# Kernel tuning notes

Hardware: AMD Instinct MI355X
Metric: run time of the kernel (lower is better)

## Reference

```python
import jax, jax.numpy as jnp
import numpy as np

# ---- config (from init_kwargs) ----
IMG_SIZE = (4096.0, 4096.0)
MAP_SIZE = (256, 256)
BASE_SIZE = 16
RATIOS = np.array([0.5, 1.0, 2.0], dtype=np.float64)
SCALES = np.array([8.0, 16.0, 32.0], dtype=np.float64)
FEAT_STRIDE = 16
RPN_MIN_SIZE = 16.0
PRE_NMS_N = 12000
POST_NMS_N = 2000
NMS_THRESH = 0.7


def _generate_anchors():
    base = np.array([1, 1, BASE_SIZE, BASE_SIZE], dtype=np.float64) - 1
    w = base[2] - base[0] + 1
    h = base[3] - base[1] + 1
    cx = base[0] + 0.5 * (w - 1)
    cy = base[1] + 0.5 * (h - 1)
    size = w * h
    ws = np.round(np.sqrt(size / RATIOS))
    hs = np.round(ws * RATIOS)
    ratio_anchors = np.stack([cx - 0.5 * (ws - 1), cy - 0.5 * (hs - 1),
                              cx + 0.5 * (ws - 1), cy + 0.5 * (hs - 1)], axis=1)
    out = []
    for a in ratio_anchors:
        aw = a[2] - a[0] + 1
        ah = a[3] - a[1] + 1
        acx = a[0] + 0.5 * (aw - 1)
        acy = a[1] + 0.5 * (ah - 1)
        ws2 = aw * SCALES
        hs2 = ah * SCALES
        out.append(np.stack([acx - 0.5 * (ws2 - 1), acy - 0.5 * (hs2 - 1),
                             acx + 0.5 * (ws2 - 1), acy + 0.5 * (hs2 - 1)], axis=1))
    return np.concatenate(out, axis=0).astype(np.float32)  # [A=9, 4]


def _all_anchors():
    A = _generate_anchors()
    H, W = MAP_SIZE
    sx = np.arange(W) * FEAT_STRIDE
    sy = np.arange(H) * FEAT_STRIDE
    sx, sy = np.meshgrid(sx, sy)
    shifts = np.stack([sx.ravel(), sy.ravel(), sx.ravel(), sy.ravel()], axis=1).astype(np.float32)  # [K,4]
    return (shifts[:, None, :] + A[None, :, :]).reshape(-1, 4)  # [K*A, 4]


_ALL_ANCHORS = _all_anchors()  # [N, 4] constant


def setup_inputs() -> dict:
    key = jax.random.key(0)
    k1, k2 = jax.random.split(key)
    n = _ALL_ANCHORS.shape[0]
    delta = jax.random.normal(k1, (1, n, 4), dtype=jnp.float32) * 0.1
    score = jax.random.uniform(k2, (1, n, 2), dtype=jnp.float32)
    return {"delta": delta, "score": score}


def _proposal_forward(delta, score):
    anchors = jnp.asarray(_ALL_ANCHORS)  # [N,4]
    d = delta[0]                         # [N,4]
    s = score[0, :, 1]                   # [N]

    widths = anchors[:, 2] - anchors[:, 0] + 1.0
    heights = anchors[:, 3] - anchors[:, 1] + 1.0
    ctr_x = anchors[:, 0] + 0.5 * widths
    ctr_y = anchors[:, 1] + 0.5 * heights
    pcx = d[:, 0] * widths + ctr_x
    pcy = d[:, 1] * heights + ctr_y
    pw = jnp.exp(d[:, 2]) * widths
    ph = jnp.exp(d[:, 3]) * heights
    x0 = jnp.clip(pcx - 0.5 * pw, 0.0, IMG_SIZE[0])
    y0 = jnp.clip(pcy - 0.5 * ph, 0.0, IMG_SIZE[1])
    x1 = jnp.clip(pcx + 0.5 * pw, 0.0, IMG_SIZE[0])
    y1 = jnp.clip(pcy + 0.5 * ph, 0.0, IMG_SIZE[1])
    props = jnp.stack([x0, y0, x1, y1], axis=1)  # [N,4]

    # min-size filter: mask instead of dynamic gather (jit-friendly)
    w = props[:, 2] - props[:, 0]
    h = props[:, 3] - props[:, 1]
    valid = (w >= RPN_MIN_SIZE) & (h >= RPN_MIN_SIZE)
    s = jnp.where(valid, s, -jnp.inf)

    top_s, top_i = jax.lax.top_k(s, PRE_NMS_N)   # sorted descending
    boxes = props[top_i]                          # [PRE,4]

    # greedy NMS over score-sorted boxes, fixed POST_NMS_N iterations
    areas = (boxes[:, 2] - boxes[:, 0]) * (boxes[:, 3] - boxes[:, 1])
    alive0 = top_s > -jnp.inf

    def step(alive, _):
        i = jnp.argmax(jnp.where(alive, top_s, -jnp.inf))
        ok = alive[i]
        b = boxes[i]
        xx0 = jnp.maximum(b[0], boxes[:, 0])
        yy0 = jnp.maximum(b[1], boxes[:, 1])
        xx1 = jnp.minimum(b[2], boxes[:, 2])
        yy1 = jnp.minimum(b[3], boxes[:, 3])
        inter = jnp.maximum(xx1 - xx0, 0.0) * jnp.maximum(yy1 - yy0, 0.0)
        iou = inter / jnp.maximum(areas[i] + areas - inter, 1e-8)
        alive = alive & (iou <= NMS_THRESH)
        out = jnp.where(ok, b, jnp.zeros_like(b))  # zero-pad like tf.pad
        return alive, out

    _, selected = jax.lax.scan(step, alive0, None, length=POST_NMS_N)  # [POST,4]
    return selected[None]  # [1, POST_NMS_N, 4]


def reference(delta, score):
    return _proposal_forward(delta, score)
```

## Files before the change

kernel.cpp:

```cpp
#include <hip/hip_runtime.h>
#include <hip/hip_bf16.h>

#define N_ANCH   589824
#define NBLK     2304
#define TOPK     12000
#define KPAD     12032
#define NW       188
#define OUTN     2000
#define CAP      32768

typedef unsigned long long u64;

__constant__ float c_aw[9] = {184.f, 368.f, 736.f, 128.f, 256.f, 512.f,  88.f, 176.f, 352.f};
__constant__ float c_ah[9] = { 96.f, 192.f, 384.f, 128.f, 256.f, 512.f, 176.f, 352.f, 704.f};

__device__ __forceinline__ void decode_one(int i, const float4* __restrict__ delta,
                                           float4* box, bool* valid) {
#pragma clang fp contract(off)
    int a    = i % 9;
    int cell = i / 9;
    int gx = cell & 255;
    int gy = cell >> 8;
    float w = c_aw[a], h = c_ah[a];
    float cx = (float)gx * 16.0f + 8.0f;
    float cy = (float)gy * 16.0f + 8.0f;
    float4 d = delta[i];
    float pcx = d.x * w + cx;
    float pcy = d.y * h + cy;
    float pw  = expf(d.z) * w;
    float ph  = expf(d.w) * h;
    float x0 = fminf(fmaxf(pcx - 0.5f * pw, 0.f), 4096.f);
    float y0 = fminf(fmaxf(pcy - 0.5f * ph, 0.f), 4096.f);
    float x1 = fminf(fmaxf(pcx + 0.5f * pw, 0.f), 4096.f);
    float y1 = fminf(fmaxf(pcy + 0.5f * ph, 0.f), 4096.f);
    *box = make_float4(x0, y0, x1, y1);
    *valid = (x1 - x0 >= 16.f) && (y1 - y0 >= 16.f);
}

__global__ __launch_bounds__(256) void k_score(const float4* __restrict__ delta,
                                               const float2* __restrict__ score,
                                               unsigned* __restrict__ ukey,
                                               unsigned* __restrict__ hist1) {
    __shared__ unsigned lh[256];
    int tid = threadIdx.x;
    lh[tid] = 0u;
    __syncthreads();
    int i = blockIdx.x * 256 + tid;
    float4 box; bool valid;
    decode_one(i, delta, &box, &valid);
    unsigned u = 0u;
    if (valid) {
        unsigned b = __float_as_uint(score[i].y);
        u = (b & 0x80000000u) ? ~b : (b | 0x80000000u);
    }
    ukey[i] = u;
    atomicAdd(&lh[u >> 24], 1u);
    __syncthreads();
    unsigned c = lh[tid];
    if (c) atomicAdd(&hist1[tid], c);
}

__global__ __launch_bounds__(256) void k_hist2(const unsigned* __restrict__ ukey,
                                               const unsigned* __restrict__ hist1,
                                               unsigned* __restrict__ hist2) {
    __shared__ unsigned ss[256];
    __shared__ unsigned lh[256];
    __shared__ unsigned s_b1;
    int tid = threadIdx.x;
    ss[tid] = hist1[tid];
    lh[tid] = 0u;
    if (tid == 0) s_b1 = 0u;
    __syncthreads();
    for (int d = 1; d < 256; d <<= 1) {
        unsigned v = (tid + d < 256) ? ss[tid + d] : 0u;
        __syncthreads();
        ss[tid] += v;
        __syncthreads();
    }
    if (ss[tid] >= (unsigned)TOPK && (tid == 255 || ss[tid + 1] < (unsigned)TOPK))
        s_b1 = (unsigned)tid;
    __syncthreads();
    unsigned b1 = s_b1;
    int i = blockIdx.x * 256 + tid;
    unsigned u = ukey[i];
    if ((u >> 24) == b1) atomicAdd(&lh[(u >> 16) & 255u], 1u);
    __syncthreads();
    unsigned c = lh[tid];
    if (c) atomicAdd(&hist2[tid], c);
}

__global__ __launch_bounds__(256) void k_compact(const unsigned* __restrict__ ukey,
                                                 const unsigned* __restrict__ hist1,
                                                 const unsigned* __restrict__ hist2,
                                                 unsigned* __restrict__ cnt,
                                                 u64* __restrict__ cand) {
    __shared__ unsigned ss[256];
    __shared__ unsigned s_b1, s_ab1, s_P;
    int tid = threadIdx.x;
    ss[tid] = hist1[tid];
    if (tid == 0) { s_b1 = 0u; s_ab1 = 0u; }
    __syncthreads();
    for (int d = 1; d < 256; d <<= 1) {
        unsigned v = (tid + d < 256) ? ss[tid + d] : 0u;
        __syncthreads();
        ss[tid] += v;
        __syncthreads();
    }
    if (ss[tid] >= (unsigned)TOPK && (tid == 255 || ss[tid + 1] < (unsigned)TOPK)) {
        s_b1 = (unsigned)tid;
        s_ab1 = (tid == 255) ? 0u : ss[tid + 1];
    }
    __syncthreads();
    unsigned b1 = s_b1, ab1 = s_ab1;
    ss[tid] = hist2[tid];
    if (tid == 0) s_P = (b1 << 8);
    __syncthreads();
    for (int d = 1; d < 256; d <<= 1) {
        unsigned v = (tid + d < 256) ? ss[tid + d] : 0u;
        __syncthreads();
        ss[tid] += v;
        __syncthreads();
    }
    unsigned target = (unsigned)TOPK - ab1;
    if (ss[tid] >= target && (tid == 255 || ss[tid + 1] < target))
        s_P = (b1 << 8) | (unsigned)tid;
    __syncthreads();
    unsigned P = s_P;

    int i = blockIdx.x * 256 + tid;
    unsigned u = ukey[i];
    bool pred = (u != 0u) && ((u >> 16) >= P);
    u64 m = __ballot(pred);
    if (m == 0ull) return;
    int lane = tid & 63;
    int leader = __ffsll(m) - 1;
    unsigned base = 0;
    if (lane == leader) base = atomicAdd(cnt, (unsigned)__popcll(m));
    base = __shfl(base, leader);
    if (pred) {
        u64 below = m & ((1ull << lane) - 1ull);
        unsigned pos = base + (unsigned)__popcll(below);
        if (pos < CAP) cand[pos] = ((u64)u << 32) | (unsigned)(~i);
    }
}

__global__ __launch_bounds__(256) void k_rankdec(const u64* __restrict__ cand,
                                                 const unsigned* __restrict__ ctrl,
                                                 const float4* __restrict__ delta,
                                                 float4* __restrict__ sboxes) {
    unsigned cnt = ctrl[3];
    int C = (int)(cnt < (unsigned)CAP ? cnt : (unsigned)CAP);
    if ((int)(blockIdx.x * 256) >= C) return;
    int t = blockIdx.x * 256 + threadIdx.x;
    u64 mykey = (t < C) ? cand[t] : ~0ull;
    int rank = 0;
    __shared__ u64 tile[256];
    for (int j0 = 0; j0 < C; j0 += 256) {
        int j = j0 + threadIdx.x;
        tile[threadIdx.x] = (j < C) ? cand[j] : 0ull;
        __syncthreads();
        int lim = (C - j0 < 256) ? (C - j0) : 256;
        #pragma unroll 4
        for (int jj = 0; jj < lim; ++jj) rank += (tile[jj] > mykey) ? 1 : 0;
        __syncthreads();
    }
    if (t < C && rank < TOPK) {
        int idx = (int)(~(unsigned)mykey);
        float4 box; bool v;
        decode_one(idx, delta, &box, &v);
        sboxes[rank] = box;
    }
}

__global__ __launch_bounds__(64) void k_mask(const float4* __restrict__ sboxes,
                                             u64* __restrict__ mcol) {
    int rb = blockIdx.y;
    int cb0 = blockIdx.x * 4;
    if (cb0 + 3 < rb) return;
    int tid = threadIdx.x;
    int r = rb * 64 + tid;
    float4 me = sboxes[r];
    float areaMe = (me.z - me.x) * (me.w - me.y);
    __shared__ float4 cbox[64];
    for (int q = 0; q < 4; ++q) {
        int cb = cb0 + q;
        if (cb < rb) continue;
        __syncthreads();
        cbox[tid] = sboxes[cb * 64 + tid];
        __syncthreads();
        u64 bits = 0ull;
        for (int j = 0; j < 64; ++j) {
            float4 o = cbox[j];
            float xx0 = fmaxf(me.x, o.x);
            float yy0 = fmaxf(me.y, o.y);
            float xx1 = fminf(me.z, o.z);
            float yy1 = fminf(me.w, o.w);
            float iw = fmaxf(xx1 - xx0, 0.f);
            float ih = fmaxf(yy1 - yy0, 0.f);
            float inter = iw * ih;
            float areaO = (o.z - o.x) * (o.w - o.y);
            float denom = fmaxf(areaMe + areaO - inter, 1e-8f);
            float iou = inter / denom;
            if (iou > 0.7f && (cb * 64 + j) != r) bits |= (1ull << j);
        }
        mcol[(size_t)cb * KPAD + r] = bits;
    }
}

__global__ __launch_bounds__(256) void k_reduce(const float4* __restrict__ sboxes,
                                                const unsigned* __restrict__ ctrl,
                                                const u64* __restrict__ mcol,
                                                float4* __restrict__ out) {
    int t = threadIdx.x;
    int lane = t & 63;
    int wave = t >> 6;
    unsigned cnt = ctrl[3];
    int C = (int)(cnt < (unsigned)CAP ? cnt : (unsigned)CAP);
    int nvalid = C < TOPK ? C : TOPK;
    int nblocks = (nvalid + 63) >> 6;

    __shared__ u64 s_rw[2];

    u64 removed_t = ~0ull;
    if (t < NW) {
        long long lo = (long long)t * 64;
        if (lo + 64 <= (long long)nvalid) removed_t = 0ull;
        else if (lo < (long long)nvalid)
            removed_t = ~((1ull << (unsigned)(nvalid - lo)) - 1ull);
    }

    int nk = 0;
    u64 p0=0,p1=0,p2=0,p3=0,p4=0,p5=0,p6=0,p7=0;
    u64 p8=0,p9=0,p10=0,p11=0,p12=0,p13=0,p14=0,p15=0;
    u64 dgnext = 0ull;
    if (nblocks > 0) dgnext = mcol[(size_t)0 * KPAD + lane];

    for (int b = 0; b < nblocks; ++b) {
        removed_t |= ((p0|p1)|(p2|p3)) | ((p4|p5)|(p6|p7));
        removed_t |= ((p8|p9)|(p10|p11)) | ((p12|p13)|(p14|p15));
        p0=p1=p2=p3=p4=p5=p6=p7=0ull;
        p8=p9=p10=p11=p12=p13=p14=p15=0ull;
        u64 dg = dgnext;
        if (t == b) s_rw[b & 1] = removed_t;
        __syncthreads();
        u64 rw = s_rw[b & 1];
        if (b + 1 < nblocks)
            dgnext = mcol[(size_t)(b + 1) * KPAD + (size_t)(b + 1) * 64 + lane];

        bool alive = ((rw >> lane) & 1ull) == 0ull;
        int budget = OUTN - nk;
        u64 keptmask = 0ull;
        int kc = 0;
        while (kc < budget) {
            u64 m = __ballot(alive);
            if (!m) break;
            int j = __ffsll(m) - 1;
            keptmask |= (1ull << j);
            ++kc;
            alive = alive && (lane != j) && (((dg >> j) & 1ull) == 0ull);
        }

        if (wave == 0 && ((keptmask >> lane) & 1ull)) {
            int pos = nk + (int)__popcll(keptmask & ((1ull << lane) - 1ull));
            out[pos] = sboxes[b * 64 + lane];
        }
        nk += kc;
        if (nk >= OUTN) break;

        if (kc > 0 && t > b && t < NW) {
            const u64* colp = mcol + (size_t)t * KPAD + (size_t)b * 64;
            u64 km = keptmask;
            int jf = __ffsll(km) - 1;
            int i0 = jf;                          km &= km - 1;
            int i1  = km ? __ffsll(km) - 1 : jf;  km &= km - 1;
            int i2  = km ? __ffsll(km) - 1 : jf;  km &= km - 1;
            int i3  = km ? __ffsll(km) - 1 : jf;  km &= km - 1;
            int i4  = km ? __ffsll(km) - 1 : jf;  km &= km - 1;
            int i5  = km ? __ffsll(km) - 1 : jf;  km &= km - 1;
            int i6  = km ? __ffsll(km) - 1 : jf;  km &= km - 1;
            int i7  = km ? __ffsll(km) - 1 : jf;  km &= km - 1;
            int i8  = km ? __ffsll(km) - 1 : jf;  km &= km - 1;
            int i9  = km ? __ffsll(km) - 1 : jf;  km &= km - 1;
            int i10 = km ? __ffsll(km) - 1 : jf;  km &= km - 1;
            int i11 = km ? __ffsll(km) - 1 : jf;  km &= km - 1;
            int i12 = km ? __ffsll(km) - 1 : jf;  km &= km - 1;
            int i13 = km ? __ffsll(km) - 1 : jf;  km &= km - 1;
            int i14 = km ? __ffsll(km) - 1 : jf;  km &= km - 1;
            int i15 = km ? __ffsll(km) - 1 : jf;  km &= km - 1;
            p0 = colp[i0];   p1 = colp[i1];   p2 = colp[i2];   p3 = colp[i3];
            p4 = colp[i4];   p5 = colp[i5];   p6 = colp[i6];   p7 = colp[i7];
            p8 = colp[i8];   p9 = colp[i9];   p10 = colp[i10]; p11 = colp[i11];
            p12 = colp[i12]; p13 = colp[i13]; p14 = colp[i14]; p15 = colp[i15];
            while (km) {
                int j = __ffsll(km) - 1; km &= km - 1;
                removed_t |= colp[j];
            }
        }
    }

    float4 z = make_float4(0.f, 0.f, 0.f, 0.f);
    for (int p = nk + t; p < OUTN; p += 256) out[p] = z;
}

extern "C" void kernel_launch(void* const* d_in, const int* in_sizes, int n_in,
                              void* d_out, int out_size, void* d_ws, size_t ws_size,
                              hipStream_t stream) {
    const float4* delta = (const float4*)d_in[0];
    const float2* score = (const float2*)d_in[1];
    char* ws = (char*)d_ws;

    unsigned* ukey  = (unsigned*)(ws + 0);
    u64*      cand  = (u64*)(ws + 2359296);
    unsigned* hist1 = (unsigned*)(ws + 2621440);
    unsigned* hist2 = (unsigned*)(ws + 2622464);
    unsigned* ctrl  = (unsigned*)(ws + 2623488);
    float4*   sbox  = (float4*)(ws + 2623552);
    u64*      mcol  = (u64*)(ws + 2816064);

    hipMemsetAsync(ws + 2621440, 0, 194624, stream);

    k_score  <<<NBLK,    256, 0, stream>>>(delta, score, ukey, hist1);
    k_hist2  <<<NBLK,    256, 0, stream>>>(ukey, hist1, hist2);
    k_compact<<<NBLK,    256, 0, stream>>>(ukey, hist1, hist2, ctrl + 3, cand);
    k_rankdec<<<CAP/256, 256, 0, stream>>>(cand, ctrl, delta, sbox);
    dim3 mgrid(47, NW);
    k_mask   <<<mgrid,   64,  0, stream>>>(sbox, mcol);
    k_reduce <<<1,       256, 0, stream>>>(sbox, ctrl, mcol, (float4*)d_out);
}
```

Before: 891.0 us.

## Fuse all proposal stages into one cooperative persistent kernel with grid syncs

```diff
diff --git a/kernel.cpp b/kernel.cpp
--- a/kernel.cpp
+++ b/kernel.cpp
@@ -1,13 +1,15 @@
 #include <hip/hip_runtime.h>
-#include <hip/hip_bf16.h>
+#include <hip/hip_cooperative_groups.h>
+
+namespace cg = cooperative_groups;
 
 #define N_ANCH   589824
-#define NBLK     2304
 #define TOPK     12000
 #define KPAD     12032
 #define NW       188
 #define OUTN     2000
 #define CAP      32768
+#define GRID     1024
 
 typedef unsigned long long u64;
 
@@ -37,39 +39,45 @@
     *valid = (x1 - x0 >= 16.f) && (y1 - y0 >= 16.f);
 }
 
-__global__ __launch_bounds__(256) void k_score(const float4* __restrict__ delta,
-                                               const float2* __restrict__ score,
-                                               unsigned* __restrict__ ukey,
-                                               unsigned* __restrict__ hist1) {
+__global__ __launch_bounds__(256, 4) void k_fused(
+        const float4* __restrict__ delta, const float2* __restrict__ score,
+        unsigned* __restrict__ ukey, unsigned* __restrict__ hist1,
+        unsigned* __restrict__ hist2, unsigned* __restrict__ ctrl,
+        u64* __restrict__ cand, float4* __restrict__ sbox,
+        u64* __restrict__ mask, float4* __restrict__ out) {
+    cg::grid_group g = cg::this_grid();
+    int tid = threadIdx.x;
+    int bid = blockIdx.x;
+    int lane = tid & 63;
+    int wave = tid >> 6;
+
     __shared__ unsigned lh[256];
-    int tid = threadIdx.x;
+    __shared__ unsigned ss[256];
+    __shared__ u64 tile[256];
+    __shared__ float4 cbox[256];
+    __shared__ unsigned s_sc[4];
+    __shared__ u64 s_rwsh[2];
+
     lh[tid] = 0u;
     __syncthreads();
-    int i = blockIdx.x * 256 + tid;
-    float4 box; bool valid;
-    decode_one(i, delta, &box, &valid);
-    unsigned u = 0u;
-    if (valid) {
-        unsigned b = __float_as_uint(score[i].y);
-        u = (b & 0x80000000u) ? ~b : (b | 0x80000000u);
-    }
-    ukey[i] = u;
-    atomicAdd(&lh[u >> 24], 1u);
-    __syncthreads();
-    unsigned c = lh[tid];
-    if (c) atomicAdd(&hist1[tid], c);
-}
-
-__global__ __launch_bounds__(256) void k_hist2(const unsigned* __restrict__ ukey,
-                                               const unsigned* __restrict__ hist1,
-                                               unsigned* __restrict__ hist2) {
-    __shared__ unsigned ss[256];
-    __shared__ unsigned lh[256];
-    __shared__ unsigned s_b1;
-    int tid = threadIdx.x;
+    for (int i = bid * 256 + tid; i < N_ANCH; i += GRID * 256) {
+        float4 box; bool valid;
+        decode_one(i, delta, &box, &valid);
+        unsigned u = 0u;
+        if (valid) {
+            unsigned b = __float_as_uint(score[i].y);
+            u = (b & 0x80000000u) ? ~b : (b | 0x80000000u);
+        }
+        ukey[i] = u;
+        atomicAdd(&lh[u >> 24], 1u);
+    }
+    __syncthreads();
+    if (lh[tid]) atomicAdd(&hist1[tid], lh[tid]);
+    g.sync();
+
     ss[tid] = hist1[tid];
     lh[tid] = 0u;
-    if (tid == 0) s_b1 = 0u;
+    if (tid == 0) s_sc[0] = 0u;
     __syncthreads();
     for (int d = 1; d < 256; d <<= 1) {
         unsigned v = (tid + d < 256) ? ss[tid + d] : 0u;
@@ -78,27 +86,19 @@
         __syncthreads();
     }
     if (ss[tid] >= (unsigned)TOPK && (tid == 255 || ss[tid + 1] < (unsigned)TOPK))
-        s_b1 = (unsigned)tid;
-    __syncthreads();
-    unsigned b1 = s_b1;
-    int i = blockIdx.x * 256 + tid;
-    unsigned u = ukey[i];
-    if ((u >> 24) == b1) atomicAdd(&lh[(u >> 16) & 255u], 1u);
-    __syncthreads();
-    unsigned c = lh[tid];
-    if (c) atomicAdd(&hist2[tid], c);
-}
-
-__global__ __launch_bounds__(256) void k_compact(const unsigned* __restrict__ ukey,
-                                                 const unsigned* __restrict__ hist1,
-                                                 const unsigned* __restrict__ hist2,
-                                                 unsigned* __restrict__ cnt,
-                                                 u64* __restrict__ cand) {
-    __shared__ unsigned ss[256];
-    __shared__ unsigned s_b1, s_ab1, s_P;
-    int tid = threadIdx.x;
+        s_sc[0] = (unsigned)tid;
+    __syncthreads();
+    unsigned b1 = s_sc[0];
+    for (int i = bid * 256 + tid; i < N_ANCH; i += GRID * 256) {
+        unsigned u = ukey[i];
+        if ((u >> 24) == b1) atomicAdd(&lh[(u >> 16) & 255u], 1u);
+    }
+    __syncthreads();
+    if (lh[tid]) atomicAdd(&hist2[tid], lh[tid]);
+    g.sync();
+
     ss[tid] = hist1[tid];
-    if (tid == 0) { s_b1 = 0u; s_ab1 = 0u; }
+    if (tid == 0) { s_sc[0] = 0u; s_sc[1] = 0u; }
     __syncthreads();
     for (int d = 1; d < 256; d <<= 1) {
         unsigned v = (tid + d < 256) ? ss[tid + d] : 0u;
@@ -107,13 +107,14 @@
         __syncthreads();
     }
     if (ss[tid] >= (unsigned)TOPK && (tid == 255 || ss[tid + 1] < (unsigned)TOPK)) {
-        s_b1 = (unsigned)tid;
-        s_ab1 = (tid == 255) ? 0u : ss[tid + 1];
-    }
-    __syncthreads();
-    unsigned b1 = s_b1, ab1 = s_ab1;
+        s_sc[0] = (unsigned)tid;
+        s_sc[1] = (tid == 255) ? 0u : ss[tid + 1];
+    }
+    __syncthreads();
+    b1 = s_sc[0];
+    unsigned ab1 = s_sc[1];
     ss[tid] = hist2[tid];
-    if (tid == 0) s_P = (b1 << 8);
+    if (tid == 0) s_sc[2] = (b1 << 8);
     __syncthreads();
     for (int d = 1; d < 256; d <<= 1) {
         unsigned v = (tid + d < 256) ? ss[tid + d] : 0u;
@@ -123,107 +124,91 @@
     }
     unsigned target = (unsigned)TOPK - ab1;
     if (ss[tid] >= target && (tid == 255 || ss[tid + 1] < target))
-        s_P = (b1 << 8) | (unsigned)tid;
-    __syncthreads();
-    unsigned P = s_P;
-
-    int i = blockIdx.x * 256 + tid;
-    unsigned u = ukey[i];
-    bool pred = (u != 0u) && ((u >> 16) >= P);
-    u64 m = __ballot(pred);
-    if (m == 0ull) return;
-    int lane = tid & 63;
-    int leader = __ffsll(m) - 1;
-    unsigned base = 0;
-    if (lane == leader) base = atomicAdd(cnt, (unsigned)__popcll(m));
-    base = __shfl(base, leader);
-    if (pred) {
-        u64 below = m & ((1ull << lane) - 1ull);
-        unsigned pos = base + (unsigned)__popcll(below);
-        if (pos < CAP) cand[pos] = ((u64)u << 32) | (unsigned)(~i);
-    }
-}
-
-__global__ __launch_bounds__(256) void k_rankdec(const u64* __restrict__ cand,
-                                                 const unsigned* __restrict__ ctrl,
-                                                 const float4* __restrict__ delta,
-                                                 float4* __restrict__ sboxes) {
+        s_sc[2] = (b1 << 8) | (unsigned)tid;
+    __syncthreads();
+    unsigned P = s_sc[2];
+    for (int i = bid * 256 + tid; i < N_ANCH; i += GRID * 256) {
+        unsigned u = ukey[i];
+        bool pred = (u != 0u) && ((u >> 16) >= P);
+        u64 m = __ballot(pred);
+        if (m) {
+            int leader = __ffsll(m) - 1;
+            unsigned base = 0;
+            if (lane == leader) base = atomicAdd(&ctrl[3], (unsigned)__popcll(m));
+            base = __shfl(base, leader);
+            if (pred) {
+                u64 below = m & ((1ull << lane) - 1ull);
+                unsigned pos = base + (unsigned)__popcll(below);
+                if (pos < CAP) cand[pos] = ((u64)u << 32) | (unsigned)(~i);
+            }
+        }
+    }
+    g.sync();
+
     unsigned cnt = ctrl[3];
     int C = (int)(cnt < (unsigned)CAP ? cnt : (unsigned)CAP);
-    if ((int)(blockIdx.x * 256) >= C) return;
-    int t = blockIdx.x * 256 + threadIdx.x;
-    u64 mykey = (t < C) ? cand[t] : ~0ull;
-    int rank = 0;
-    __shared__ u64 tile[256];
-    for (int j0 = 0; j0 < C; j0 += 256) {
-        int j = j0 + threadIdx.x;
-        tile[threadIdx.x] = (j < C) ? cand[j] : 0ull;
-        __syncthreads();
-        int lim = (C - j0 < 256) ? (C - j0) : 256;
-        #pragma unroll 4
-        for (int jj = 0; jj < lim; ++jj) rank += (tile[jj] > mykey) ? 1 : 0;
-        __syncthreads();
-    }
-    if (t < C && rank < TOPK) {
-        int idx = (int)(~(unsigned)mykey);
-        float4 box; bool v;
-        decode_one(idx, delta, &box, &v);
-        sboxes[rank] = box;
-    }
-}
-
-__global__ __launch_bounds__(64) void k_mask(const float4* __restrict__ sboxes,
-                                             u64* __restrict__ mcol) {
-    int rb = blockIdx.y;
-    int cb0 = blockIdx.x * 4;
-    if (cb0 + 3 < rb) return;
-    int tid = threadIdx.x;
-    int r = rb * 64 + tid;
-    float4 me = sboxes[r];
-    float areaMe = (me.z - me.x) * (me.w - me.y);
-    __shared__ float4 cbox[64];
-    for (int q = 0; q < 4; ++q) {
-        int cb = cb0 + q;
-        if (cb < rb) continue;
-        __syncthreads();
-        cbox[tid] = sboxes[cb * 64 + tid];
-        __syncthreads();
-        u64 bits = 0ull;
-        for (int j = 0; j < 64; ++j) {
-            float4 o = cbox[j];
-            float xx0 = fmaxf(me.x, o.x);
-            float yy0 = fmaxf(me.y, o.y);
-            float xx1 = fminf(me.z, o.z);
-            float yy1 = fminf(me.w, o.w);
-            float iw = fmaxf(xx1 - xx0, 0.f);
-            float ih = fmaxf(yy1 - yy0, 0.f);
-            float inter = iw * ih;
-            float areaO = (o.z - o.x) * (o.w - o.y);
-            float denom = fmaxf(areaMe + areaO - inter, 1e-8f);
-            float iou = inter / denom;
-            if (iou > 0.7f && (cb * 64 + j) != r) bits |= (1ull << j);
-        }
-        mcol[(size_t)cb * KPAD + r] = bits;
-    }
-}
-
-__global__ __launch_bounds__(256) void k_reduce(const float4* __restrict__ sboxes,
-                                                const unsigned* __restrict__ ctrl,
-                                                const u64* __restrict__ mcol,
-                                                float4* __restrict__ out) {
-    int t = threadIdx.x;
-    int lane = t & 63;
-    int wave = t >> 6;
-    unsigned cnt = ctrl[3];
-    int C = (int)(cnt < (unsigned)CAP ? cnt : (unsigned)CAP);
+    if (bid * 256 < C) {
+        int t = bid * 256 + tid;
+        u64 mykey = (t < C) ? cand[t] : ~0ull;
+        int rank = 0;
+        for (int j0 = 0; j0 < C; j0 += 256) {
+            int j = j0 + tid;
+            tile[tid] = (j < C) ? cand[j] : 0ull;
+            __syncthreads();
+            int lim = (C - j0 < 256) ? (C - j0) : 256;
+            #pragma unroll 4
+            for (int jj = 0; jj < lim; ++jj) rank += (tile[jj] > mykey) ? 1 : 0;
+            __syncthreads();
+        }
+        if (t < C && rank < TOPK) {
+            int idx = (int)(~(unsigned)mykey);
+            float4 box; bool v;
+            decode_one(idx, delta, &box, &v);
+            sbox[rank] = box;
+        }
+    }
+    g.sync();
+
+    for (unsigned tix = (unsigned)bid; tix < 47u * 188u; tix += GRID) {
+        int rb = (int)(tix / 47u);
+        int cb0 = (int)(tix % 47u) * 4;
+        if (cb0 + 3 < rb) continue;
+        __syncthreads();
+        cbox[tid] = sbox[cb0 * 64 + tid];
+        __syncthreads();
+        int cb = cb0 + wave;
+        if (cb >= rb) {
+            int r = rb * 64 + lane;
+            float4 me = sbox[r];
+            float areaMe = (me.z - me.x) * (me.w - me.y);
+            u64 bits = 0ull;
+            for (int j = 0; j < 64; ++j) {
+                float4 o = cbox[wave * 64 + j];
+                float xx0 = fmaxf(me.x, o.x);
+                float yy0 = fmaxf(me.y, o.y);
+                float xx1 = fminf(me.z, o.z);
+                float yy1 = fminf(me.w, o.w);
+                float iw = fmaxf(xx1 - xx0, 0.f);
+                float ih = fmaxf(yy1 - yy0, 0.f);
+                float inter = iw * ih;
+                float areaO = (o.z - o.x) * (o.w - o.y);
+                float denom = fmaxf(areaMe + areaO - inter, 1e-8f);
+                float iou = inter / denom;
+                if (iou > 0.7f && (cb * 64 + j) != r) bits |= (1ull << j);
+            }
+            mask[(size_t)r * NW + cb] = bits;
+        }
+    }
+    g.sync();
+
+    if (bid != 0) return;
+
     int nvalid = C < TOPK ? C : TOPK;
     int nblocks = (nvalid + 63) >> 6;
 
-    __shared__ u64 s_rw[2];
-
     u64 removed_t = ~0ull;
-    if (t < NW) {
-        long long lo = (long long)t * 64;
+    if (tid < NW) {
+        long long lo = (long long)tid * 64;
         if (lo + 64 <= (long long)nvalid) removed_t = 0ull;
         else if (lo < (long long)nvalid)
             removed_t = ~((1ull << (unsigned)(nvalid - lo)) - 1ull);
@@ -233,7 +218,7 @@
     u64 p0=0,p1=0,p2=0,p3=0,p4=0,p5=0,p6=0,p7=0;
     u64 p8=0,p9=0,p10=0,p11=0,p12=0,p13=0,p14=0,p15=0;
     u64 dgnext = 0ull;
-    if (nblocks > 0) dgnext = mcol[(size_t)0 * KPAD + lane];
+    if (nblocks > 0) dgnext = mask[(size_t)lane * NW + 0];
 
     for (int b = 0; b < nblocks; ++b) {
         removed_t |= ((p0|p1)|(p2|p3)) | ((p4|p5)|(p6|p7));
@@ -241,11 +226,11 @@
         p0=p1=p2=p3=p4=p5=p6=p7=0ull;
         p8=p9=p10=p11=p12=p13=p14=p15=0ull;
         u64 dg = dgnext;
-        if (t == b) s_rw[b & 1] = removed_t;
-        __syncthreads();
-        u64 rw = s_rw[b & 1];
+        if (tid == b) s_rwsh[b & 1] = removed_t;
+        __syncthreads();
+        u64 rw = s_rwsh[b & 1];
         if (b + 1 < nblocks)
-            dgnext = mcol[(size_t)(b + 1) * KPAD + (size_t)(b + 1) * 64 + lane];
+            dgnext = mask[(size_t)((b + 1) * 64 + lane) * NW + (b + 1)];
 
         bool alive = ((rw >> lane) & 1ull) == 0ull;
         int budget = OUTN - nk;
@@ -262,13 +247,13 @@
 
         if (wave == 0 && ((keptmask >> lane) & 1ull)) {
             int pos = nk + (int)__popcll(keptmask & ((1ull << lane) - 1ull));
-            out[pos] = sboxes[b * 64 + lane];
+            out[pos] = sbox[b * 64 + lane];
         }
         nk += kc;
         if (nk >= OUTN) break;
 
-        if (kc > 0 && t > b && t < NW) {
-            const u64* colp = mcol + (size_t)t * KPAD + (size_t)b * 64;
+        if (kc > 0 && tid > b && tid < NW) {
+            const u64* mt = mask + tid;
             u64 km = keptmask;
             int jf = __ffsll(km) - 1;
             int i0 = jf;                          km &= km - 1;
@@ -287,19 +272,32 @@
             int i13 = km ? __ffsll(km) - 1 : jf;  km &= km - 1;
             int i14 = km ? __ffsll(km) - 1 : jf;  km &= km - 1;
             int i15 = km ? __ffsll(km) - 1 : jf;  km &= km - 1;
-            p0 = colp[i0];   p1 = colp[i1];   p2 = colp[i2];   p3 = colp[i3];
-            p4 = colp[i4];   p5 = colp[i5];   p6 = colp[i6];   p7 = colp[i7];
-            p8 = colp[i8];   p9 = colp[i9];   p10 = colp[i10]; p11 = colp[i11];
-            p12 = colp[i12]; p13 = colp[i13]; p14 = colp[i14]; p15 = colp[i15];
+            size_t rb8 = (size_t)b * 64 * NW;
+            p0  = mt[rb8 + (size_t)i0  * NW];
+            p1  = mt[rb8 + (size_t)i1  * NW];
+            p2  = mt[rb8 + (size_t)i2  * NW];
+            p3  = mt[rb8 + (size_t)i3  * NW];
+            p4  = mt[rb8 + (size_t)i4  * NW];
+            p5  = mt[rb8 + (size_t)i5  * NW];
+            p6  = mt[rb8 + (size_t)i6  * NW];
+            p7  = mt[rb8 + (size_t)i7  * NW];
+            p8  = mt[rb8 + (size_t)i8  * NW];
+            p9  = mt[rb8 + (size_t)i9  * NW];
+            p10 = mt[rb8 + (size_t)i10 * NW];
+            p11 = mt[rb8 + (size_t)i11 * NW];
+            p12 = mt[rb8 + (size_t)i12 * NW];
+            p13 = mt[rb8 + (size_t)i13 * NW];
+            p14 = mt[rb8 + (size_t)i14 * NW];
+            p15 = mt[rb8 + (size_t)i15 * NW];
             while (km) {
                 int j = __ffsll(km) - 1; km &= km - 1;
-                removed_t |= colp[j];
+                removed_t |= mt[rb8 + (size_t)j * NW];
             }
         }
     }
 
     float4 z = make_float4(0.f, 0.f, 0.f, 0.f);
-    for (int p = nk + t; p < OUTN; p += 256) out[p] = z;
+    for (int p = nk + tid; p < OUTN; p += 256) out[p] = z;
 }
 
 extern "C" void kernel_launch(void* const* d_in, const int* in_sizes, int n_in,
@@ -315,15 +313,13 @@
     unsigned* hist2 = (unsigned*)(ws + 2622464);
     unsigned* ctrl  = (unsigned*)(ws + 2623488);
     float4*   sbox  = (float4*)(ws + 2623552);
-    u64*      mcol  = (u64*)(ws + 2816064);
+    u64*      mask  = (u64*)(ws + 2816064);
+    float4*   outp  = (float4*)d_out;
 
     hipMemsetAsync(ws + 2621440, 0, 194624, stream);
 
-    k_score  <<<NBLK,    256, 0, stream>>>(delta, score, ukey, hist1);
-    k_hist2  <<<NBLK,    256, 0, stream>>>(ukey, hist1, hist2);
-    k_compact<<<NBLK,    256, 0, stream>>>(ukey, hist1, hist2, ctrl + 3, cand);
-    k_rankdec<<<CAP/256, 256, 0, stream>>>(cand, ctrl, delta, sbox);
-    dim3 mgrid(47, NW);
-    k_mask   <<<mgrid,   64,  0, stream>>>(sbox, mcol);
-    k_reduce <<<1,       256, 0, stream>>>(sbox, ctrl, mcol, (float4*)d_out);
+    void* args[] = {&delta, &score, &ukey, &hist1, &hist2, &ctrl,
+                    &cand, &sbox, &mask, &outp};
+    hipLaunchCooperativeKernel((const void*)k_fused, dim3(GRID), dim3(256),
+                               args, 0, stream);
 }
```

New measurement: 1.410 ms. 58.3% more time.
